# Optimization experiments

Measured on AMD Instinct MI355X. Metric: run time of the kernel, lower is better.

The kernel has to match this reference:

```python
import jax, jax.numpy as jnp
import numpy as np


def _gcn_conv(x, W, b, src, dst, num_nodes):
    """PyG GCNConv with default args: add self-loops + symmetric normalization.
    x: [N, F_in], W: [F_in, F_out], b: [F_out], src/dst: [E] (self-loops already included).
    """
    h = x @ W  # [N, F_out]
    # in-degree of destination nodes (counting self-loops)
    ones = jnp.ones_like(dst, dtype=h.dtype)
    deg = jax.ops.segment_sum(ones, dst, num_segments=num_nodes)  # [N]
    dinv = jnp.where(deg > 0, jax.lax.rsqrt(jnp.maximum(deg, 1.0)), 0.0)
    norm = dinv[src] * dinv[dst]  # [E]
    msgs = h[src] * norm[:, None]  # [E, F_out] gather + scale
    out = jax.ops.segment_sum(msgs, dst, num_segments=num_nodes)  # scatter-add
    return out + b


def setup_inputs() -> dict:
    key = jax.random.key(0)
    k1, k2, k3, k4 = jax.random.split(key, 4)
    N, E, F_IN, HID = 100000, 1600000, 128, 64
    x = jax.random.normal(k1, (N, F_IN), dtype=jnp.float32)
    edge_index = jax.random.randint(k2, (2, E), 0, N, dtype=jnp.int64)
    W1 = jax.random.normal(k3, (F_IN, HID), dtype=jnp.float32) * (1.0 / np.sqrt(F_IN))
    b1 = jnp.zeros((HID,), dtype=jnp.float32)
    W2 = jax.random.normal(k4, (HID, 1), dtype=jnp.float32) * (1.0 / np.sqrt(HID))
    b2 = jnp.zeros((1,), dtype=jnp.float32)
    return {"x": x, "edge_index": edge_index, "W1": W1, "b1": b1, "W2": W2, "b2": b2}


def reference(x, edge_index, W1, b1, W2, b2):
    N = x.shape[0]
    # add self-loops (GCNConv default add_self_loops=True)
    loop = jnp.arange(N, dtype=edge_index.dtype)
    src = jnp.concatenate([edge_index[0], loop])
    dst = jnp.concatenate([edge_index[1], loop])
    h = jax.nn.relu(_gcn_conv(x, W1, b1, src, dst, N))
    out = _gcn_conv(h, W2, b2, src, dst, N)
    return out  # [N, 1]
```

## Files before the change

kernel.cpp:

```cpp
#include <hip/hip_runtime.h>
#include <hip/hip_fp16.h>

#define F_IN 128
#define HID  64
#define CAP  96
#define CSHIFT 9
#define CNODES 512
#define NC_MAX 256
#define CCHUNK 4096
#define BCAPC 8960

__launch_bounds__(256)
__global__ void k_coarse(const int* __restrict__ src, const int* __restrict__ dst,
                         int* __restrict__ acur, int* __restrict__ ent, int E, int nc) {
    __shared__ int s_cnt[NC_MAX];
    __shared__ int s_gb[NC_MAX];
    __shared__ int s_bump[NC_MAX];
    int t = threadIdx.x;
    int e0 = blockIdx.x * CCHUNK;
    int n = E - e0; if (n > CCHUNK) n = CCHUNK;

    for (int i = t; i < nc; i += 256) { s_cnt[i] = 0; s_bump[i] = 0; }
    __syncthreads();
    for (int i = t; i < n; i += 256)
        atomicAdd(&s_cnt[dst[e0 + i] >> CSHIFT], 1);
    __syncthreads();
    if (t < nc) {
        int c = s_cnt[t];
        s_gb[t] = (c > 0) ? atomicAdd(&acur[t], c) : 0;
    }
    __syncthreads();
    for (int i = t; i < n; i += 256) {
        int d = dst[e0 + i], s = src[e0 + i];
        int b = d >> CSHIFT;
        int p = s_gb[b] + atomicAdd(&s_bump[b], 1);
        if (p < BCAPC) ent[(size_t)b * BCAPC + p] = (s << CSHIFT) | (d & (CNODES - 1));
    }
}

__launch_bounds__(1024)
__global__ void k_fillc(const int* __restrict__ acur, const int* __restrict__ ent,
                        int* __restrict__ counts, int* __restrict__ csrc, int N) {
    __shared__ int lcnt[CNODES];
    int b = blockIdx.x, t = threadIdx.x;
    if (t < CNODES) lcnt[t] = 0;
    __syncthreads();
    int base = b * CNODES;
    int cnt = acur[b]; if (cnt > BCAPC) cnt = BCAPC;
    const int* ep = ent + (size_t)b * BCAPC;
    for (int i = t; i < cnt; i += 1024) {
        int v = ep[i];
        int ld = v & (CNODES - 1), s = v >> CSHIFT;
        int p = atomicAdd(&lcnt[ld], 1);
        if (p < CAP) csrc[(size_t)(base + ld) * CAP + p] = s;
    }
    __syncthreads();
    if (t < CNODES && base + t < N) {
        int cc = lcnt[t]; if (cc > CAP) cc = CAP;
        counts[base + t] = cc;
    }
}

#define SX 65
__launch_bounds__(256, 4)
__global__ void k_gemm(const float* __restrict__ x, const float* __restrict__ W1,
                       const int* __restrict__ counts, __half* __restrict__ hn, int N) {
    __shared__ float xT[F_IN * SX];
    int t = threadIdx.x;
    int r0 = blockIdx.x * 64;

    const float4* xg = (const float4*)(x + (size_t)r0 * F_IN);
    int maxf = (N - r0) * (F_IN / 4);
#pragma unroll
    for (int j = 0; j < 8; ++j) {
        int f = t + j * 256;
        int row = f >> 5;
        int k0  = (f & 31) * 4;
        float4 v = (f < maxf) ? xg[f] : make_float4(0.f, 0.f, 0.f, 0.f);
        xT[(k0 + 0) * SX + row] = v.x;
        xT[(k0 + 1) * SX + row] = v.y;
        xT[(k0 + 2) * SX + row] = v.z;
        xT[(k0 + 3) * SX + row] = v.w;
    }
    __syncthreads();

    int lane = t & 63;
    int c0 = __builtin_amdgcn_readfirstlane(t >> 6) * 16;
    int row = r0 + lane;

    float acc[16];
#pragma unroll
    for (int c = 0; c < 16; ++c) acc[c] = 0.f;

    for (int k = 0; k < F_IN; k += 4) {
        float x0 = xT[(k + 0) * SX + lane];
        float x1 = xT[(k + 1) * SX + lane];
        float x2 = xT[(k + 2) * SX + lane];
        float x3 = xT[(k + 3) * SX + lane];
        const float* wr = W1 + (size_t)k * HID + c0;
#pragma unroll
        for (int c = 0; c < 16; ++c) {
            float a = acc[c];
            a = fmaf(x0, wr[c], a);
            a = fmaf(x1, wr[HID + c], a);
            a = fmaf(x2, wr[2 * HID + c], a);
            a = fmaf(x3, wr[3 * HID + c], a);
            acc[c] = a;
        }
    }

    if (row < N) {
        float di = rsqrtf((float)(counts[row] + 1));
        __half* hp = hn + (size_t)row * HID + c0;
        unsigned int us[8];
#pragma unroll
        for (int c = 0; c < 16; c += 2) {
            __half2 h2 = __floats2half2_rn(acc[c] * di, acc[c + 1] * di);
            us[c >> 1] = *(unsigned int*)&h2;
        }
        *(uint4*)&hp[0] = make_uint4(us[0], us[1], us[2], us[3]);
        *(uint4*)&hp[8] = make_uint4(us[4], us[5], us[6], us[7]);
    }
}

__device__ inline float4 ldh4(const __half* p) {
    int2 raw = *(const int2*)p;
    __half2 a = *(__half2*)&raw.x, b = *(__half2*)&raw.y;
    float2 fa = __half22float2(a), fb = __half22float2(b);
    return make_float4(fa.x, fa.y, fb.x, fb.y);
}

__launch_bounds__(256)
__global__ void k_gather1(const int* __restrict__ csrc, const int* __restrict__ counts,
                          const __half* __restrict__ hn, const float* __restrict__ b1,
                          const float* __restrict__ W2, float* __restrict__ zn, int N) {
    int lane = threadIdx.x & 63;
    int r = blockIdx.x * 4 + (threadIdx.x >> 6);
    if (r >= N) return;
    int g  = lane >> 4;
    int li = lane & 15;
    size_t beg = (size_t)r * CAP;
    int cnt = counts[r];

    float4 a0 = make_float4(0.f, 0.f, 0.f, 0.f);
    float4 a1 = make_float4(0.f, 0.f, 0.f, 0.f);
    int j = g;
    for (; j + 4 < cnt; j += 8) {
        int s0 = csrc[beg + j];
        int s1 = csrc[beg + j + 4];
        float4 h0 = ldh4(&hn[(size_t)s0 * HID + li * 4]);
        float4 h1 = ldh4(&hn[(size_t)s1 * HID + li * 4]);
        a0.x += h0.x; a0.y += h0.y; a0.z += h0.z; a0.w += h0.w;
        a1.x += h1.x; a1.y += h1.y; a1.z += h1.z; a1.w += h1.w;
    }
    if (j < cnt) {
        int s0 = csrc[beg + j];
        float4 h0 = ldh4(&hn[(size_t)s0 * HID + li * 4]);
        a0.x += h0.x; a0.y += h0.y; a0.z += h0.z; a0.w += h0.w;
    }
    a0.x += a1.x; a0.y += a1.y; a0.z += a1.z; a0.w += a1.w;

    a0.x += __shfl_xor(a0.x, 16, 64); a0.y += __shfl_xor(a0.y, 16, 64);
    a0.z += __shfl_xor(a0.z, 16, 64); a0.w += __shfl_xor(a0.w, 16, 64);
    a0.x += __shfl_xor(a0.x, 32, 64); a0.y += __shfl_xor(a0.y, 32, 64);
    a0.z += __shfl_xor(a0.z, 32, 64); a0.w += __shfl_xor(a0.w, 32, 64);

    float di = rsqrtf((float)(cnt + 1));
    float4 hr = ldh4(&hn[(size_t)r * HID + li * 4]);
    float4 bv = *(const float4*)&b1[li * 4];
    float4 wv = *(const float4*)&W2[li * 4];
    float vx = fmaxf(di * (a0.x + hr.x) + bv.x, 0.f);
    float vy = fmaxf(di * (a0.y + hr.y) + bv.y, 0.f);
    float vz = fmaxf(di * (a0.z + hr.z) + bv.z, 0.f);
    float vw = fmaxf(di * (a0.w + hr.w) + bv.w, 0.f);
    float p = vx * wv.x + vy * wv.y + vz * wv.z + vw * wv.w;
    p += __shfl_xor(p, 1, 64);
    p += __shfl_xor(p, 2, 64);
    p += __shfl_xor(p, 4, 64);
    p += __shfl_xor(p, 8, 64);
    if (lane == 0) zn[r] = p * di;
}

__global__ void k_gather2(const int* __restrict__ csrc, const int* __restrict__ counts,
                          const float* __restrict__ zn, const float* __restrict__ b2,
                          float* __restrict__ out, int N) {
    int t = blockIdx.x * blockDim.x + threadIdx.x;
    int r = t >> 4, li = t & 15;
    if (r >= N) return;
    size_t beg = (size_t)r * CAP;
    int cnt = counts[r];
    float acc = 0.f;
    for (int j = li; j < cnt; j += 16) {
        acc += zn[csrc[beg + j]];
    }
    acc += __shfl_xor(acc, 1, 64);
    acc += __shfl_xor(acc, 2, 64);
    acc += __shfl_xor(acc, 4, 64);
    acc += __shfl_xor(acc, 8, 64);
    if (li == 0) {
        float di = rsqrtf((float)(cnt + 1));
        out[r] = di * (acc + zn[r]) + b2[0];
    }
}

extern "C" void kernel_launch(void* const* d_in, const int* in_sizes, int n_in,
                              void* d_out, int out_size, void* d_ws, size_t ws_size,
                              hipStream_t stream) {
    const float* x  = (const float*)d_in[0];
    const int*   ei = (const int*)d_in[1];
    const float* W1 = (const float*)d_in[2];
    const float* b1 = (const float*)d_in[3];
    const float* W2 = (const float*)d_in[4];
    const float* b2 = (const float*)d_in[5];
    float* out = (float*)d_out;

    const int N = in_sizes[0] / F_IN;
    const int E = in_sizes[1] / 2;
    const int* src = ei;
    const int* dst = ei + E;

    const int nc = (N + CNODES - 1) / CNODES;
    const int NBKT = (N + 63) / 64;

    char* ws = (char*)d_ws;
    size_t off = 0;
    auto alloc = [&](size_t bytes) { void* p = ws + off; off += (bytes + 255) & ~255ULL; return p; };
    int*    acur   = (int*)   alloc((size_t)nc * 4);
    int*    counts = (int*)   alloc((size_t)N * 4);
    float*  zn     = (float*) alloc((size_t)N * 4);
    int*    ent    = (int*)   alloc((size_t)nc * BCAPC * 4);
    __half* hn     = (__half*)alloc((size_t)N * HID * 2);
    int*    csrc   = (int*)   alloc((size_t)N * CAP * 4);

    hipMemsetAsync(acur, 0, (size_t)nc * 4, stream);

    const int coarseBlks = (E + CCHUNK - 1) / CCHUNK;
    k_coarse<<<coarseBlks, 256, 0, stream>>>(src, dst, acur, ent, E, nc);
    k_fillc<<<nc, 1024, 0, stream>>>(acur, ent, counts, csrc, N);
    k_gemm<<<NBKT, 256, 0, stream>>>(x, W1, counts, hn, N);
    k_gather1<<<(N + 3) / 4, 256, 0, stream>>>(csrc, counts, hn, b1, W2, zn, N);
    k_gather2<<<((size_t)N * 16 + 255) / 256, 256, 0, stream>>>(csrc, counts, zn, b2, out, N);
}
```

Baseline: 218.2 us.

## Make gather1 persistent with prefetched neighbor indices and 16-byte row loads

The first-layer gather kernel becomes a grid-stride persistent kernel with 2048 blocks. Each wave prefetches the next row's count and neighbor indices into registers and broadcasts them with shuffles, instead of having every lane group reload csrc. Each lane now loads 8 halves (16 bytes) per neighbor, with 8 neighbors in flight per iteration, which widens memory transactions and overlaps index fetch with the feature gather. The price is more register pressure, a fixed grid size, and a slow fallback path for rows with more than 64 neighbors.

```diff
diff --git a/kernel.cpp b/kernel.cpp
--- a/kernel.cpp
+++ b/kernel.cpp
@@ -123,11 +123,15 @@
     }
 }
 
-__device__ inline float4 ldh4(const __half* p) {
-    int2 raw = *(const int2*)p;
-    __half2 a = *(__half2*)&raw.x, b = *(__half2*)&raw.y;
-    float2 fa = __half22float2(a), fb = __half22float2(b);
-    return make_float4(fa.x, fa.y, fb.x, fb.y);
+__device__ inline void acc8(float a[8], int4 raw) {
+    int v[4] = { raw.x, raw.y, raw.z, raw.w };
+#pragma unroll
+    for (int k = 0; k < 4; ++k) {
+        __half2 h2 = *(__half2*)&v[k];
+        float2 f = __half22float2(h2);
+        a[2 * k]     += f.x;
+        a[2 * k + 1] += f.y;
+    }
 }
 
 __launch_bounds__(256)
@@ -135,50 +139,95 @@
                           const __half* __restrict__ hn, const float* __restrict__ b1,
                           const float* __restrict__ W2, float* __restrict__ zn, int N) {
     int lane = threadIdx.x & 63;
-    int r = blockIdx.x * 4 + (threadIdx.x >> 6);
+    int li   = lane & 7;
+    int g    = lane >> 3;
+    int wave = blockIdx.x * 4 + (threadIdx.x >> 6);
+    int nW   = gridDim.x * 4;
+
+    int r = wave;
     if (r >= N) return;
-    int g  = lane >> 4;
-    int li = lane & 15;
-    size_t beg = (size_t)r * CAP;
-    int cnt = counts[r];
-
-    float4 a0 = make_float4(0.f, 0.f, 0.f, 0.f);
-    float4 a1 = make_float4(0.f, 0.f, 0.f, 0.f);
-    int j = g;
-    for (; j + 4 < cnt; j += 8) {
-        int s0 = csrc[beg + j];
-        int s1 = csrc[beg + j + 4];
-        float4 h0 = ldh4(&hn[(size_t)s0 * HID + li * 4]);
-        float4 h1 = ldh4(&hn[(size_t)s1 * HID + li * 4]);
-        a0.x += h0.x; a0.y += h0.y; a0.z += h0.z; a0.w += h0.w;
-        a1.x += h1.x; a1.y += h1.y; a1.z += h1.z; a1.w += h1.w;
-    }
-    if (j < cnt) {
-        int s0 = csrc[beg + j];
-        float4 h0 = ldh4(&hn[(size_t)s0 * HID + li * 4]);
-        a0.x += h0.x; a0.y += h0.y; a0.z += h0.z; a0.w += h0.w;
-    }
-    a0.x += a1.x; a0.y += a1.y; a0.z += a1.z; a0.w += a1.w;
-
-    a0.x += __shfl_xor(a0.x, 16, 64); a0.y += __shfl_xor(a0.y, 16, 64);
-    a0.z += __shfl_xor(a0.z, 16, 64); a0.w += __shfl_xor(a0.w, 16, 64);
-    a0.x += __shfl_xor(a0.x, 32, 64); a0.y += __shfl_xor(a0.y, 32, 64);
-    a0.z += __shfl_xor(a0.z, 32, 64); a0.w += __shfl_xor(a0.w, 32, 64);
-
-    float di = rsqrtf((float)(cnt + 1));
-    float4 hr = ldh4(&hn[(size_t)r * HID + li * 4]);
-    float4 bv = *(const float4*)&b1[li * 4];
-    float4 wv = *(const float4*)&W2[li * 4];
-    float vx = fmaxf(di * (a0.x + hr.x) + bv.x, 0.f);
-    float vy = fmaxf(di * (a0.y + hr.y) + bv.y, 0.f);
-    float vz = fmaxf(di * (a0.z + hr.z) + bv.z, 0.f);
-    float vw = fmaxf(di * (a0.w + hr.w) + bv.w, 0.f);
-    float p = vx * wv.x + vy * wv.y + vz * wv.z + vw * wv.w;
-    p += __shfl_xor(p, 1, 64);
-    p += __shfl_xor(p, 2, 64);
-    p += __shfl_xor(p, 4, 64);
-    p += __shfl_xor(p, 8, 64);
-    if (lane == 0) zn[r] = p * di;
+
+    float4 bv0 = *(const float4*)&b1[li * 8];
+    float4 bv1 = *(const float4*)&b1[li * 8 + 4];
+    float4 wv0 = *(const float4*)&W2[li * 8];
+    float4 wv1 = *(const float4*)&W2[li * 8 + 4];
+
+    int cnt  = counts[r];
+    int sIdx = (lane < cnt) ? csrc[(size_t)r * CAP + lane] : -1;
+
+    while (r < N) {
+        int rn = r + nW;
+        int cntn = 0, sIdxn = -1;
+        if (rn < N) {
+            cntn = counts[rn];
+            if (lane < cntn) sIdxn = csrc[(size_t)rn * CAP + lane];
+        }
+
+        float a[8];
+#pragma unroll
+        for (int k = 0; k < 8; ++k) a[k] = 0.f;
+
+        int cEff = cnt > 64 ? 64 : cnt;
+        int nIt  = (cEff + 7) >> 3;
+
+        int it = 0;
+        for (; it + 2 <= nIt; it += 2) {
+            int e0 = it * 8 + g;
+            int e1 = e0 + 8;
+            int s0 = __shfl(sIdx, e0, 64);
+            int s1 = __shfl(sIdx, e1, 64);
+            bool p1 = (e1 < cEff);
+            int4 r0 = *(const int4*)&hn[(size_t)s0 * HID + li * 8];
+            int4 r1;
+            if (p1) r1 = *(const int4*)&hn[(size_t)s1 * HID + li * 8];
+            acc8(a, r0);
+            if (p1) acc8(a, r1);
+        }
+        if (it < nIt) {
+            int e0 = it * 8 + g;
+            int s0 = __shfl(sIdx, e0, 64);
+            if (e0 < cEff) {
+                int4 r0 = *(const int4*)&hn[(size_t)s0 * HID + li * 8];
+                acc8(a, r0);
+            }
+        }
+        if (cnt > 64) {
+            size_t beg = (size_t)r * CAP;
+            for (int e = 64 + g; e < cnt; e += 8) {
+                int s = csrc[beg + e];
+                int4 rv = *(const int4*)&hn[(size_t)s * HID + li * 8];
+                acc8(a, rv);
+            }
+        }
+
+#pragma unroll
+        for (int k = 0; k < 8; ++k) {
+            a[k] += __shfl_xor(a[k], 8, 64);
+            a[k] += __shfl_xor(a[k], 16, 64);
+            a[k] += __shfl_xor(a[k], 32, 64);
+        }
+
+        int4 rawr = *(const int4*)&hn[(size_t)r * HID + li * 8];
+        acc8(a, rawr);
+
+        float di = rsqrtf((float)(cnt + 1));
+        float v0 = fmaxf(fmaf(di, a[0], bv0.x), 0.f);
+        float v1 = fmaxf(fmaf(di, a[1], bv0.y), 0.f);
+        float v2 = fmaxf(fmaf(di, a[2], bv0.z), 0.f);
+        float v3 = fmaxf(fmaf(di, a[3], bv0.w), 0.f);
+        float v4 = fmaxf(fmaf(di, a[4], bv1.x), 0.f);
+        float v5 = fmaxf(fmaf(di, a[5], bv1.y), 0.f);
+        float v6 = fmaxf(fmaf(di, a[6], bv1.z), 0.f);
+        float v7 = fmaxf(fmaf(di, a[7], bv1.w), 0.f);
+        float p = v0 * wv0.x + v1 * wv0.y + v2 * wv0.z + v3 * wv0.w
+                + v4 * wv1.x + v5 * wv1.y + v6 * wv1.z + v7 * wv1.w;
+        p += __shfl_xor(p, 1, 64);
+        p += __shfl_xor(p, 2, 64);
+        p += __shfl_xor(p, 4, 64);
+        if (lane == 0) zn[r] = p * di;
+
+        r = rn; cnt = cntn; sIdx = sIdxn;
+    }
 }
 
 __global__ void k_gather2(const int* __restrict__ csrc, const int* __restrict__ counts,
@@ -238,6 +287,6 @@
     k_coarse<<<coarseBlks, 256, 0, stream>>>(src, dst, acur, ent, E, nc);
     k_fillc<<<nc, 1024, 0, stream>>>(acur, ent, counts, csrc, N);
     k_gemm<<<NBKT, 256, 0, stream>>>(x, W1, counts, hn, N);
-    k_gather1<<<(N + 3) / 4, 256, 0, stream>>>(csrc, counts, hn, b1, W2, zn, N);
+    k_gather1<<<2048, 256, 0, stream>>>(csrc, counts, hn, b1, W2, zn, N);
     k_gather2<<<((size_t)N * 16 + 255) / 256, 256, 0, stream>>>(csrc, counts, zn, b2, out, N);
 }
```

Result: slower. 225.3 us (+3.3%).

## Restructure layer-1 gather: two rows per wave, 16-byte loads, batched neighbor fetches

Applied to the files above, without the earlier changes.

The first-layer gather kernel now maps two destination rows to each 64-lane wave, with 8 lanes per row slice each loading 16 bytes (8 halves) instead of 8 bytes. Neighbor indices are read as int4 vectors and four row loads are issued together per lane, with masking through zero weights instead of branches, so more memory requests are in flight. It is meant to raise memory-level parallelism and reduce instruction overhead in the gather. The cost is some wasted loads for padded slots and loop trip counts set by the larger count of the two rows sharing a wave.

```diff
diff --git a/kernel.cpp b/kernel.cpp
--- a/kernel.cpp
+++ b/kernel.cpp
@@ -123,11 +123,15 @@
     }
 }
 
-__device__ inline float4 ldh4(const __half* p) {
-    int2 raw = *(const int2*)p;
-    __half2 a = *(__half2*)&raw.x, b = *(__half2*)&raw.y;
-    float2 fa = __half22float2(a), fb = __half22float2(b);
-    return make_float4(fa.x, fa.y, fb.x, fb.y);
+__device__ inline void accum8(float acc[8], int4 raw, float w) {
+    int v[4] = { raw.x, raw.y, raw.z, raw.w };
+#pragma unroll
+    for (int h = 0; h < 4; ++h) {
+        __half2 h2 = *(__half2*)&v[h];
+        float2 f = __half22float2(h2);
+        acc[2 * h]     = fmaf(w, f.x, acc[2 * h]);
+        acc[2 * h + 1] = fmaf(w, f.y, acc[2 * h + 1]);
+    }
 }
 
 __launch_bounds__(256)
@@ -135,50 +139,108 @@
                           const __half* __restrict__ hn, const float* __restrict__ b1,
                           const float* __restrict__ W2, float* __restrict__ zn, int N) {
     int lane = threadIdx.x & 63;
-    int r = blockIdx.x * 4 + (threadIdx.x >> 6);
-    if (r >= N) return;
-    int g  = lane >> 4;
-    int li = lane & 15;
-    size_t beg = (size_t)r * CAP;
-    int cnt = counts[r];
-
-    float4 a0 = make_float4(0.f, 0.f, 0.f, 0.f);
-    float4 a1 = make_float4(0.f, 0.f, 0.f, 0.f);
-    int j = g;
-    for (; j + 4 < cnt; j += 8) {
-        int s0 = csrc[beg + j];
-        int s1 = csrc[beg + j + 4];
-        float4 h0 = ldh4(&hn[(size_t)s0 * HID + li * 4]);
-        float4 h1 = ldh4(&hn[(size_t)s1 * HID + li * 4]);
-        a0.x += h0.x; a0.y += h0.y; a0.z += h0.z; a0.w += h0.w;
-        a1.x += h1.x; a1.y += h1.y; a1.z += h1.z; a1.w += h1.w;
-    }
-    if (j < cnt) {
-        int s0 = csrc[beg + j];
-        float4 h0 = ldh4(&hn[(size_t)s0 * HID + li * 4]);
-        a0.x += h0.x; a0.y += h0.y; a0.z += h0.z; a0.w += h0.w;
-    }
-    a0.x += a1.x; a0.y += a1.y; a0.z += a1.z; a0.w += a1.w;
-
-    a0.x += __shfl_xor(a0.x, 16, 64); a0.y += __shfl_xor(a0.y, 16, 64);
-    a0.z += __shfl_xor(a0.z, 16, 64); a0.w += __shfl_xor(a0.w, 16, 64);
-    a0.x += __shfl_xor(a0.x, 32, 64); a0.y += __shfl_xor(a0.y, 32, 64);
-    a0.z += __shfl_xor(a0.z, 32, 64); a0.w += __shfl_xor(a0.w, 32, 64);
+    int g    = (lane >> 3) & 3;
+    int li   = lane & 7;
+    int r = blockIdx.x * 8 + ((threadIdx.x >> 6) << 1) + (lane >> 5);
+    int rr = (r < N) ? r : (N - 1);
+    int cnt = (r < N) ? counts[rr] : 0;
+
+    const int4* cs4 = (const int4*)(csrc + (size_t)rr * CAP);
+    size_t lo = (size_t)li * 8;
+
+    float acc[8];
+#pragma unroll
+    for (int c = 0; c < 8; ++c) acc[c] = 0.f;
+
+    {
+        int4 sA = cs4[g];
+        int idx[4]; float w[4];
+        idx[0] = sA.x; idx[1] = sA.y; idx[2] = sA.z; idx[3] = sA.w;
+#pragma unroll
+        for (int k = 0; k < 4; ++k) {
+            int e = 4 * g + k;
+            bool v = (e < cnt);
+            idx[k] = v ? idx[k] : rr;
+            w[k]   = v ? 1.f : 0.f;
+        }
+        int4 raw[4];
+#pragma unroll
+        for (int k = 0; k < 4; ++k)
+            raw[k] = *(const int4*)&hn[(size_t)idx[k] * HID + lo];
+#pragma unroll
+        for (int k = 0; k < 4; ++k) accum8(acc, raw[k], w[k]);
+    }
+
+    int cntO = __shfl_xor(cnt, 32, 64);
+    int cmax = (cnt > cntO) ? cnt : cntO;
+
+    if (cmax > 16) {
+        int4 sB = cs4[4 + g];
+        int idx[4]; float w[4];
+        idx[0] = sB.x; idx[1] = sB.y; idx[2] = sB.z; idx[3] = sB.w;
+#pragma unroll
+        for (int k = 0; k < 4; ++k) {
+            int e = 16 + 4 * g + k;
+            bool v = (e < cnt);
+            idx[k] = v ? idx[k] : rr;
+            w[k]   = v ? 1.f : 0.f;
+        }
+        int4 raw[4];
+#pragma unroll
+        for (int k = 0; k < 4; ++k)
+            raw[k] = *(const int4*)&hn[(size_t)idx[k] * HID + lo];
+#pragma unroll
+        for (int k = 0; k < 4; ++k) accum8(acc, raw[k], w[k]);
+    }
+
+    for (int c = 32; c < cmax; c += 16) {
+        int4 s = cs4[(c >> 2) + g];
+        int idx[4]; float w[4];
+        idx[0] = s.x; idx[1] = s.y; idx[2] = s.z; idx[3] = s.w;
+#pragma unroll
+        for (int k = 0; k < 4; ++k) {
+            int e = c + 4 * g + k;
+            bool v = (e < cnt);
+            idx[k] = v ? idx[k] : rr;
+            w[k]   = v ? 1.f : 0.f;
+        }
+        int4 raw[4];
+#pragma unroll
+        for (int k = 0; k < 4; ++k)
+            raw[k] = *(const int4*)&hn[(size_t)idx[k] * HID + lo];
+#pragma unroll
+        for (int k = 0; k < 4; ++k) accum8(acc, raw[k], w[k]);
+    }
+
+#pragma unroll
+    for (int c = 0; c < 8; ++c) {
+        acc[c] += __shfl_xor(acc[c], 8, 64);
+        acc[c] += __shfl_xor(acc[c], 16, 64);
+    }
+
+    int4 rawR = *(const int4*)&hn[(size_t)rr * HID + lo];
+    accum8(acc, rawR, 1.f);
 
     float di = rsqrtf((float)(cnt + 1));
-    float4 hr = ldh4(&hn[(size_t)r * HID + li * 4]);
-    float4 bv = *(const float4*)&b1[li * 4];
-    float4 wv = *(const float4*)&W2[li * 4];
-    float vx = fmaxf(di * (a0.x + hr.x) + bv.x, 0.f);
-    float vy = fmaxf(di * (a0.y + hr.y) + bv.y, 0.f);
-    float vz = fmaxf(di * (a0.z + hr.z) + bv.z, 0.f);
-    float vw = fmaxf(di * (a0.w + hr.w) + bv.w, 0.f);
-    float p = vx * wv.x + vy * wv.y + vz * wv.z + vw * wv.w;
+    float4 b0 = *(const float4*)&b1[li * 8];
+    float4 b4 = *(const float4*)&b1[li * 8 + 4];
+    float4 w0 = *(const float4*)&W2[li * 8];
+    float4 w4 = *(const float4*)&W2[li * 8 + 4];
+
+    float p = fmaxf(fmaf(di, acc[0], b0.x), 0.f) * w0.x
+            + fmaxf(fmaf(di, acc[1], b0.y), 0.f) * w0.y
+            + fmaxf(fmaf(di, acc[2], b0.z), 0.f) * w0.z
+            + fmaxf(fmaf(di, acc[3], b0.w), 0.f) * w0.w
+            + fmaxf(fmaf(di, acc[4], b4.x), 0.f) * w4.x
+            + fmaxf(fmaf(di, acc[5], b4.y), 0.f) * w4.y
+            + fmaxf(fmaf(di, acc[6], b4.z), 0.f) * w4.z
+            + fmaxf(fmaf(di, acc[7], b4.w), 0.f) * w4.w;
+
     p += __shfl_xor(p, 1, 64);
     p += __shfl_xor(p, 2, 64);
     p += __shfl_xor(p, 4, 64);
-    p += __shfl_xor(p, 8, 64);
-    if (lane == 0) zn[r] = p * di;
+
+    if ((lane & 31) == 0 && r < N) zn[r] = p * di;
 }
 
 __global__ void k_gather2(const int* __restrict__ csrc, const int* __restrict__ counts,
@@ -238,6 +300,6 @@
     k_coarse<<<coarseBlks, 256, 0, stream>>>(src, dst, acur, ent, E, nc);
     k_fillc<<<nc, 1024, 0, stream>>>(acur, ent, counts, csrc, N);
     k_gemm<<<NBKT, 256, 0, stream>>>(x, W1, counts, hn, N);
-    k_gather1<<<(N + 3) / 4, 256, 0, stream>>>(csrc, counts, hn, b1, W2, zn, N);
+    k_gather1<<<(N + 7) / 8, 256, 0, stream>>>(csrc, counts, hn, b1, W2, zn, N);
     k_gather2<<<((size_t)N * 16 + 255) / 256, 256, 0, stream>>>(csrc, counts, zn, b2, out, N);
 }
```

Measured after the change: 197.8 us. 1.1x faster.
